# Optimization experiments

Hardware: AMD Instinct MI355X
Metric: run time of the kernel (lower is better)

Reference implementation:

```python
import jax, jax.numpy as jnp
import numpy as np

B = 32768          # batch (replay-buffer minibatch)
OBS, ACT = 17, 6   # HalfCheetah-style dims
IN = OBS + ACT
H = 256            # hidden width hard-coded in the module
N = 10             # num_q_nets


def setup_inputs() -> dict:
    key = jax.random.key(0)
    ks = jax.random.split(key, 8)
    # PyTorch Linear default init: U(-1/sqrt(fan_in), 1/sqrt(fan_in)); scale randn similarly.
    s1, s2, s3 = 1.0 / np.sqrt(IN), 1.0 / np.sqrt(H), 1.0 / np.sqrt(H)
    return {
        "state": jax.random.normal(ks[0], (B, OBS), dtype=jnp.float32),
        "action": jax.random.uniform(ks[1], (B, ACT), dtype=jnp.float32, minval=-1.0, maxval=1.0),
        "W1": jax.random.normal(ks[2], (N, IN, H), dtype=jnp.float32) * s1,
        "b1": jax.random.normal(ks[3], (N, H), dtype=jnp.float32) * s1,
        "W2": jax.random.normal(ks[4], (N, H, H), dtype=jnp.float32) * s2,
        "b2": jax.random.normal(ks[5], (N, H), dtype=jnp.float32) * s2,
        "W3": jax.random.normal(ks[6], (N, H, 1), dtype=jnp.float32) * s3,
        "b3": jax.random.normal(ks[7], (N, 1), dtype=jnp.float32) * s3,
    }


def reference(state, action, W1, b1, W2, b2, W3, b3):
    # x: [B, OBS+ACT]
    x = jnp.concatenate([state, action], axis=1)
    # batched-over-ensemble GEMMs; n=ensemble member, b=batch
    h1 = jax.nn.relu(jnp.einsum("bi,nih->nbh", x, W1) + b1[:, None, :])   # [N,B,H]
    h2 = jax.nn.relu(jnp.einsum("nbh,nho->nbo", h1, W2) + b2[:, None, :])  # [N,B,H]
    out = jnp.einsum("nbh,nho->nbo", h2, W3) + b3[:, None, :]              # [N,B,1]
    return out
```

## Files before the change

kernel.cpp:

```cpp
#include <hip/hip_runtime.h>
#include <hip/hip_bf16.h>


typedef __attribute__((ext_vector_type(8))) short bf16x8;
typedef __attribute__((ext_vector_type(4))) float f32x4;

#define B_TOTAL 32768
#define NQ 10
#define HDIM 256
#define BT 128
#define XS_STRIDE 40
#define H_STRIDE 264

#define W1P_ELEMS (NQ * 16 * 64 * 8)
#define W2P_ELEMS (NQ * 8 * 16 * 64 * 8)
#define W3P_ELEMS (NQ * 8 * 64 * 8)

__device__ __forceinline__ unsigned short f2bf(float f) {
  unsigned int u = __float_as_uint(f);
  u = u + 0x7FFFu + ((u >> 16) & 1u);
  return (unsigned short)(u >> 16);
}

__device__ __forceinline__ unsigned int pk2bf(float a, float b) {
  union { __hip_bfloat162 h; unsigned int u; } cv;
  cv.h = __float22bfloat162_rn(make_float2(a, b));
  return cv.u;
}

__global__ void pack_weights_kernel(const float* __restrict__ W1,
                                    const float* __restrict__ W2,
                                    const float* __restrict__ W3,
                                    unsigned short* __restrict__ w1p,
                                    unsigned short* __restrict__ w2p,
                                    unsigned short* __restrict__ w3p) {
  int t = blockIdx.x * 256 + threadIdx.x;
  const int NW1 = NQ * 16 * 64;
  const int NW2 = NQ * 8 * 16 * 64;
  if (t < NW1) {
    int lane = t & 63, mt = (t >> 6) & 15, n = t >> 10;
    int m = lane & 15, q = lane >> 4;
    int outc = mt * 16 + m;
#pragma unroll
    for (int j = 0; j < 8; j++) {
      int k = q * 8 + j;
      float v = (k < 23) ? W1[(n * 23 + k) * 256 + outc] : 0.f;
      w1p[(size_t)t * 8 + j] = f2bf(v);
    }
  } else if (t < NW1 + NW2) {
    int u = t - NW1;
    int lane = u & 63, mt = (u >> 6) & 15, kt = (u >> 10) & 7, n = u >> 13;
    int m = lane & 15, q = lane >> 4;
    int outc = mt * 16 + m;
#pragma unroll
    for (int j = 0; j < 8; j++) {
      int h = kt * 32 + q * 8 + j;
      w2p[(size_t)u * 8 + j] = f2bf(W2[((size_t)(n * 256 + h)) * 256 + outc]);
    }
  } else {
    int u = t - NW1 - NW2;
    int lane = u & 63, kt = (u >> 6) & 7, n = u >> 9;
    int m = lane & 15, q = lane >> 4;
#pragma unroll
    for (int j = 0; j < 8; j++) {
      int h = kt * 32 + q * 8 + j;
      float v = (m == 0) ? W3[n * 256 + h] : 0.f;
      w3p[(size_t)u * 8 + j] = f2bf(v);
    }
  }
}

__global__ __launch_bounds__(256, 2) void fused_ensemble_kernel(
    const float* __restrict__ state,
    const float* __restrict__ action,
    const unsigned short* __restrict__ w1p,
    const float* __restrict__ b1,
    const unsigned short* __restrict__ w2p,
    const float* __restrict__ b2,
    const unsigned short* __restrict__ w3p,
    const float* __restrict__ b3,
    float* __restrict__ out) {
  __shared__ __align__(16) unsigned short xs[BT * XS_STRIDE];
  __shared__ __align__(16) unsigned short hs[BT * H_STRIDE];

  const int tid = threadIdx.x;
  const int lane = tid & 63;
  const int wave = tid >> 6;
  const int m = lane & 15;
  const int q = lane >> 4;

  const int n = blockIdx.x >> 8;
  const int tile = blockIdx.x & 255;
  const int row0 = tile * BT;

  {
    const float* sp = state + (size_t)row0 * 17;
    for (int i = tid; i < BT * 17; i += 256) {
      int b = i / 17, k = i - b * 17;
      xs[b * XS_STRIDE + k] = f2bf(sp[i]);
    }
    const float* ap = action + (size_t)row0 * 6;
    for (int i = tid; i < BT * 6; i += 256) {
      int b = i / 6, k = i - b * 6;
      xs[b * XS_STRIDE + 17 + k] = f2bf(ap[i]);
    }
    for (int i = tid; i < BT * 9; i += 256) {
      int b = i / 9, k = i - b * 9;
      xs[b * XS_STRIDE + 23 + k] = 0;
    }
  }
  __syncthreads();

  f32x4 acc[4][8];

  {
    bf16x8 afrag[4];
#pragma unroll
    for (int mt = 0; mt < 4; mt++)
      afrag[mt] = *(const bf16x8*)(w1p + (((size_t)n * 16 + wave * 4 + mt) * 64 + lane) * 8);
#pragma unroll
    for (int mt = 0; mt < 4; mt++) {
      float4 bv = *(const float4*)&b1[n * HDIM + (wave * 4 + mt) * 16 + q * 4];
      f32x4 bi = (f32x4){bv.x, bv.y, bv.z, bv.w};
#pragma unroll
      for (int nt = 0; nt < 8; nt++) acc[mt][nt] = bi;
    }
#pragma unroll
    for (int nt = 0; nt < 8; nt++) {
      bf16x8 bfrag = *(const bf16x8*)&xs[(nt * 16 + m) * XS_STRIDE + q * 8];
#pragma unroll
      for (int mt = 0; mt < 4; mt++)
        acc[mt][nt] = __builtin_amdgcn_mfma_f32_16x16x32_bf16(afrag[mt], bfrag, acc[mt][nt], 0, 0, 0);
    }
  }

#pragma unroll
  for (int mt = 0; mt < 4; mt++)
#pragma unroll
    for (int nt = 0; nt < 8; nt++) {
      f32x4 a = acc[mt][nt];
      uint2 w;
      w.x = pk2bf(fmaxf(a[0], 0.f), fmaxf(a[1], 0.f));
      w.y = pk2bf(fmaxf(a[2], 0.f), fmaxf(a[3], 0.f));
      *(uint2*)&hs[(nt * 16 + m) * H_STRIDE + (wave * 4 + mt) * 16 + q * 4] = w;
    }
  __syncthreads();

  {
    const unsigned short* w2n = w2p + (size_t)n * (8 * 16 * 64 * 8);
    bf16x8 acur[4], anxt[4];
#pragma unroll
    for (int mt = 0; mt < 4; mt++)
      acur[mt] = *(const bf16x8*)(w2n + (((size_t)(wave * 4 + mt)) * 64 + lane) * 8);
#pragma unroll
    for (int mt = 0; mt < 4; mt++) {
      float4 bv = *(const float4*)&b2[n * HDIM + (wave * 4 + mt) * 16 + q * 4];
      f32x4 bi = (f32x4){bv.x, bv.y, bv.z, bv.w};
#pragma unroll
      for (int nt = 0; nt < 8; nt++) acc[mt][nt] = bi;
    }
#pragma unroll
    for (int kt = 0; kt < 8; kt++) {
      if (kt < 7) {
#pragma unroll
        for (int mt = 0; mt < 4; mt++)
          anxt[mt] = *(const bf16x8*)(w2n + (((size_t)(kt + 1) * 16 + wave * 4 + mt) * 64 + lane) * 8);
      }
      bf16x8 bfrag[8];
#pragma unroll
      for (int nt = 0; nt < 8; nt++)
        bfrag[nt] = *(const bf16x8*)&hs[(nt * 16 + m) * H_STRIDE + kt * 32 + q * 8];
#pragma unroll
      for (int nt = 0; nt < 8; nt++)
#pragma unroll
        for (int mt = 0; mt < 4; mt++)
          acc[mt][nt] = __builtin_amdgcn_mfma_f32_16x16x32_bf16(acur[mt], bfrag[nt], acc[mt][nt], 0, 0, 0);
#pragma unroll
      for (int mt = 0; mt < 4; mt++) acur[mt] = anxt[mt];
    }
  }
  __syncthreads();

#pragma unroll
  for (int mt = 0; mt < 4; mt++)
#pragma unroll
    for (int nt = 0; nt < 8; nt++) {
      f32x4 a = acc[mt][nt];
      uint2 w;
      w.x = pk2bf(fmaxf(a[0], 0.f), fmaxf(a[1], 0.f));
      w.y = pk2bf(fmaxf(a[2], 0.f), fmaxf(a[3], 0.f));
      *(uint2*)&hs[(nt * 16 + m) * H_STRIDE + (wave * 4 + mt) * 16 + q * 4] = w;
    }
  __syncthreads();

  {
    const unsigned short* w3n = w3p + (size_t)n * (8 * 64 * 8);
    f32x4 acc3[2];
    acc3[0] = (f32x4){0.f, 0.f, 0.f, 0.f};
    acc3[1] = (f32x4){0.f, 0.f, 0.f, 0.f};
#pragma unroll
    for (int kt = 0; kt < 8; kt++) {
      bf16x8 af = *(const bf16x8*)(w3n + ((size_t)kt * 64 + lane) * 8);
#pragma unroll
      for (int i = 0; i < 2; i++) {
        bf16x8 bf_ = *(const bf16x8*)&hs[((wave * 2 + i) * 16 + m) * H_STRIDE + kt * 32 + q * 8];
        acc3[i] = __builtin_amdgcn_mfma_f32_16x16x32_bf16(af, bf_, acc3[i], 0, 0, 0);
      }
    }
    if (lane < 16) {
      float bias = b3[n];
#pragma unroll
      for (int i = 0; i < 2; i++)
        out[(size_t)n * B_TOTAL + row0 + (wave * 2 + i) * 16 + m] = acc3[i][0] + bias;
    }
  }
}

extern "C" void kernel_launch(void* const* d_in, const int* in_sizes, int n_in,
                              void* d_out, int out_size, void* d_ws, size_t ws_size,
                              hipStream_t stream) {
  const float* state  = (const float*)d_in[0];
  const float* action = (const float*)d_in[1];
  const float* W1 = (const float*)d_in[2];
  const float* b1 = (const float*)d_in[3];
  const float* W2 = (const float*)d_in[4];
  const float* b2 = (const float*)d_in[5];
  const float* W3 = (const float*)d_in[6];
  const float* b3 = (const float*)d_in[7];
  float* out = (float*)d_out;

  unsigned short* w1p = (unsigned short*)d_ws;
  unsigned short* w2p = (unsigned short*)((char*)d_ws + (size_t)W1P_ELEMS * 2);
  unsigned short* w3p = (unsigned short*)((char*)d_ws + (size_t)(W1P_ELEMS + W2P_ELEMS) * 2);

  pack_weights_kernel<<<380, 256, 0, stream>>>(W1, W2, W3, w1p, w2p, w3p);
  fused_ensemble_kernel<<<NQ * (B_TOTAL / BT), 256, 0, stream>>>(
      state, action, w1p, b1, w2p, b2, w3p, b3, out);
}
```

Before: 132.5 us.

## Fuse layer-3 dot product into layer-2 epilogue and use 8 waves per block

Layer 3 is now computed straight from the layer-2 accumulators: ReLU, an FMA against fp32 W3, and a cross-lane plus cross-wave reduction through shared memory. This drops the second hidden-state write to LDS, its barrier, and the padded layer-3 MFMA pass. Blocks grow to 512 threads (8 waves, 2 M-tiles each), which halves the accumulator registers per wave and targets higher occupancy. The hidden LDS buffer uses a k-quad-major layout so that MFMA B-fragment reads are contiguous, and the pack kernel writes vectorized 16-byte stores and no longer packs W3.

```diff
diff --git a/kernel.cpp b/kernel.cpp
--- a/kernel.cpp
+++ b/kernel.cpp
@@ -10,11 +10,9 @@
 #define HDIM 256
 #define BT 128
 #define XS_STRIDE 40
-#define H_STRIDE 264
 
 #define W1P_ELEMS (NQ * 16 * 64 * 8)
 #define W2P_ELEMS (NQ * 8 * 16 * 64 * 8)
-#define W3P_ELEMS (NQ * 8 * 64 * 8)
 
 __device__ __forceinline__ unsigned short f2bf(float f) {
   unsigned int u = __float_as_uint(f);
@@ -30,131 +28,124 @@
 
 __global__ void pack_weights_kernel(const float* __restrict__ W1,
                                     const float* __restrict__ W2,
-                                    const float* __restrict__ W3,
                                     unsigned short* __restrict__ w1p,
-                                    unsigned short* __restrict__ w2p,
-                                    unsigned short* __restrict__ w3p) {
+                                    unsigned short* __restrict__ w2p) {
   int t = blockIdx.x * 256 + threadIdx.x;
   const int NW1 = NQ * 16 * 64;
-  const int NW2 = NQ * 8 * 16 * 64;
   if (t < NW1) {
     int lane = t & 63, mt = (t >> 6) & 15, n = t >> 10;
     int m = lane & 15, q = lane >> 4;
     int outc = mt * 16 + m;
+    unsigned short v[8];
 #pragma unroll
     for (int j = 0; j < 8; j++) {
       int k = q * 8 + j;
-      float v = (k < 23) ? W1[(n * 23 + k) * 256 + outc] : 0.f;
-      w1p[(size_t)t * 8 + j] = f2bf(v);
-    }
-  } else if (t < NW1 + NW2) {
+      v[j] = (k < 23) ? f2bf(W1[(n * 23 + k) * 256 + outc]) : (unsigned short)0;
+    }
+    *(uint4*)&w1p[(size_t)t * 8] = *(const uint4*)v;
+  } else {
     int u = t - NW1;
     int lane = u & 63, mt = (u >> 6) & 15, kt = (u >> 10) & 7, n = u >> 13;
     int m = lane & 15, q = lane >> 4;
     int outc = mt * 16 + m;
+    unsigned short v[8];
 #pragma unroll
     for (int j = 0; j < 8; j++) {
       int h = kt * 32 + q * 8 + j;
-      w2p[(size_t)u * 8 + j] = f2bf(W2[((size_t)(n * 256 + h)) * 256 + outc]);
-    }
-  } else {
-    int u = t - NW1 - NW2;
-    int lane = u & 63, kt = (u >> 6) & 7, n = u >> 9;
-    int m = lane & 15, q = lane >> 4;
-#pragma unroll
-    for (int j = 0; j < 8; j++) {
-      int h = kt * 32 + q * 8 + j;
-      float v = (m == 0) ? W3[n * 256 + h] : 0.f;
-      w3p[(size_t)u * 8 + j] = f2bf(v);
-    }
-  }
-}
-
-__global__ __launch_bounds__(256, 2) void fused_ensemble_kernel(
+      v[j] = f2bf(W2[((size_t)(n * 256 + h)) * 256 + outc]);
+    }
+    *(uint4*)&w2p[(size_t)u * 8] = *(const uint4*)v;
+  }
+}
+
+__global__ __launch_bounds__(512, 4) void fused_ensemble_kernel(
     const float* __restrict__ state,
     const float* __restrict__ action,
     const unsigned short* __restrict__ w1p,
     const float* __restrict__ b1,
     const unsigned short* __restrict__ w2p,
     const float* __restrict__ b2,
-    const unsigned short* __restrict__ w3p,
+    const float* __restrict__ W3,
     const float* __restrict__ b3,
     float* __restrict__ out) {
   __shared__ __align__(16) unsigned short xs[BT * XS_STRIDE];
-  __shared__ __align__(16) unsigned short hs[BT * H_STRIDE];
+  __shared__ __align__(16) unsigned short hs[32 * BT * 8];
 
   const int tid = threadIdx.x;
   const int lane = tid & 63;
-  const int wave = tid >> 6;
+  const int w = tid >> 6;
   const int m = lane & 15;
   const int q = lane >> 4;
 
   const int n = blockIdx.x >> 8;
-  const int tile = blockIdx.x & 255;
-  const int row0 = tile * BT;
+  const int row0 = (blockIdx.x & 255) * BT;
 
   {
     const float* sp = state + (size_t)row0 * 17;
-    for (int i = tid; i < BT * 17; i += 256) {
+    for (int i = tid; i < BT * 17; i += 512) {
       int b = i / 17, k = i - b * 17;
       xs[b * XS_STRIDE + k] = f2bf(sp[i]);
     }
     const float* ap = action + (size_t)row0 * 6;
-    for (int i = tid; i < BT * 6; i += 256) {
+    for (int i = tid; i < BT * 6; i += 512) {
       int b = i / 6, k = i - b * 6;
       xs[b * XS_STRIDE + 17 + k] = f2bf(ap[i]);
     }
-    for (int i = tid; i < BT * 9; i += 256) {
+    for (int i = tid; i < BT * 9; i += 512) {
       int b = i / 9, k = i - b * 9;
       xs[b * XS_STRIDE + 23 + k] = 0;
     }
   }
   __syncthreads();
 
-  f32x4 acc[4][8];
-
-  {
-    bf16x8 afrag[4];
-#pragma unroll
-    for (int mt = 0; mt < 4; mt++)
-      afrag[mt] = *(const bf16x8*)(w1p + (((size_t)n * 16 + wave * 4 + mt) * 64 + lane) * 8);
-#pragma unroll
-    for (int mt = 0; mt < 4; mt++) {
-      float4 bv = *(const float4*)&b1[n * HDIM + (wave * 4 + mt) * 16 + q * 4];
+  f32x4 acc[2][8];
+
+  {
+    bf16x8 af[2];
+#pragma unroll
+    for (int mt = 0; mt < 2; mt++)
+      af[mt] = *(const bf16x8*)(w1p + (((size_t)n * 16 + w * 2 + mt) * 64 + lane) * 8);
+#pragma unroll
+    for (int mt = 0; mt < 2; mt++) {
+      float4 bv = *(const float4*)&b1[n * HDIM + (w * 2 + mt) * 16 + q * 4];
       f32x4 bi = (f32x4){bv.x, bv.y, bv.z, bv.w};
 #pragma unroll
       for (int nt = 0; nt < 8; nt++) acc[mt][nt] = bi;
     }
 #pragma unroll
     for (int nt = 0; nt < 8; nt++) {
-      bf16x8 bfrag = *(const bf16x8*)&xs[(nt * 16 + m) * XS_STRIDE + q * 8];
-#pragma unroll
-      for (int mt = 0; mt < 4; mt++)
-        acc[mt][nt] = __builtin_amdgcn_mfma_f32_16x16x32_bf16(afrag[mt], bfrag, acc[mt][nt], 0, 0, 0);
-    }
-  }
-
-#pragma unroll
-  for (int mt = 0; mt < 4; mt++)
-#pragma unroll
-    for (int nt = 0; nt < 8; nt++) {
-      f32x4 a = acc[mt][nt];
-      uint2 w;
-      w.x = pk2bf(fmaxf(a[0], 0.f), fmaxf(a[1], 0.f));
-      w.y = pk2bf(fmaxf(a[2], 0.f), fmaxf(a[3], 0.f));
-      *(uint2*)&hs[(nt * 16 + m) * H_STRIDE + (wave * 4 + mt) * 16 + q * 4] = w;
-    }
+      bf16x8 bfr = *(const bf16x8*)&xs[(nt * 16 + m) * XS_STRIDE + q * 8];
+#pragma unroll
+      for (int mt = 0; mt < 2; mt++)
+        acc[mt][nt] = __builtin_amdgcn_mfma_f32_16x16x32_bf16(af[mt], bfr, acc[mt][nt], 0, 0, 0);
+    }
+  }
+
+  {
+    const int kqb = w * 4 + (q >> 1);
+    const int joff = (q & 1) * 4;
+#pragma unroll
+    for (int mt = 0; mt < 2; mt++)
+#pragma unroll
+      for (int nt = 0; nt < 8; nt++) {
+        f32x4 a = acc[mt][nt];
+        uint2 wv;
+        wv.x = pk2bf(fmaxf(a[0], 0.f), fmaxf(a[1], 0.f));
+        wv.y = pk2bf(fmaxf(a[2], 0.f), fmaxf(a[3], 0.f));
+        *(uint2*)&hs[(((kqb + mt * 2) * BT) + nt * 16 + m) * 8 + joff] = wv;
+      }
+  }
   __syncthreads();
 
   {
     const unsigned short* w2n = w2p + (size_t)n * (8 * 16 * 64 * 8);
-    bf16x8 acur[4], anxt[4];
-#pragma unroll
-    for (int mt = 0; mt < 4; mt++)
-      acur[mt] = *(const bf16x8*)(w2n + (((size_t)(wave * 4 + mt)) * 64 + lane) * 8);
-#pragma unroll
-    for (int mt = 0; mt < 4; mt++) {
-      float4 bv = *(const float4*)&b2[n * HDIM + (wave * 4 + mt) * 16 + q * 4];
+    bf16x8 acur[2], anxt[2];
+#pragma unroll
+    for (int mt = 0; mt < 2; mt++)
+      acur[mt] = *(const bf16x8*)(w2n + (((size_t)(w * 2 + mt)) * 64 + lane) * 8);
+#pragma unroll
+    for (int mt = 0; mt < 2; mt++) {
+      float4 bv = *(const float4*)&b2[n * HDIM + (w * 2 + mt) * 16 + q * 4];
       f32x4 bi = (f32x4){bv.x, bv.y, bv.z, bv.w};
 #pragma unroll
       for (int nt = 0; nt < 8; nt++) acc[mt][nt] = bi;
@@ -163,55 +154,62 @@
     for (int kt = 0; kt < 8; kt++) {
       if (kt < 7) {
 #pragma unroll
-        for (int mt = 0; mt < 4; mt++)
-          anxt[mt] = *(const bf16x8*)(w2n + (((size_t)(kt + 1) * 16 + wave * 4 + mt) * 64 + lane) * 8);
-      }
-      bf16x8 bfrag[8];
-#pragma unroll
-      for (int nt = 0; nt < 8; nt++)
-        bfrag[nt] = *(const bf16x8*)&hs[(nt * 16 + m) * H_STRIDE + kt * 32 + q * 8];
-#pragma unroll
-      for (int nt = 0; nt < 8; nt++)
-#pragma unroll
-        for (int mt = 0; mt < 4; mt++)
-          acc[mt][nt] = __builtin_amdgcn_mfma_f32_16x16x32_bf16(acur[mt], bfrag[nt], acc[mt][nt], 0, 0, 0);
-#pragma unroll
-      for (int mt = 0; mt < 4; mt++) acur[mt] = anxt[mt];
-    }
-  }
-  __syncthreads();
-
-#pragma unroll
-  for (int mt = 0; mt < 4; mt++)
+        for (int mt = 0; mt < 2; mt++)
+          anxt[mt] = *(const bf16x8*)(w2n + (((size_t)(kt + 1) * 16 + w * 2 + mt) * 64 + lane) * 8);
+      }
+#pragma unroll
+      for (int half = 0; half < 2; half++) {
+        bf16x8 bfr[4];
+#pragma unroll
+        for (int i = 0; i < 4; i++) {
+          int nt = half * 4 + i;
+          bfr[i] = *(const bf16x8*)&hs[((kt * 4 + q) * BT + nt * 16 + m) * 8];
+        }
+#pragma unroll
+        for (int i = 0; i < 4; i++)
+#pragma unroll
+          for (int mt = 0; mt < 2; mt++)
+            acc[mt][half * 4 + i] = __builtin_amdgcn_mfma_f32_16x16x32_bf16(
+                acur[mt], bfr[i], acc[mt][half * 4 + i], 0, 0, 0);
+      }
+#pragma unroll
+      for (int mt = 0; mt < 2; mt++) acur[mt] = anxt[mt];
+    }
+  }
+
+  {
+    float4 w3v[2];
+#pragma unroll
+    for (int mt = 0; mt < 2; mt++)
+      w3v[mt] = *(const float4*)&W3[n * HDIM + (w * 2 + mt) * 16 + q * 4];
+    float p[8];
 #pragma unroll
     for (int nt = 0; nt < 8; nt++) {
-      f32x4 a = acc[mt][nt];
-      uint2 w;
-      w.x = pk2bf(fmaxf(a[0], 0.f), fmaxf(a[1], 0.f));
-      w.y = pk2bf(fmaxf(a[2], 0.f), fmaxf(a[3], 0.f));
-      *(uint2*)&hs[(nt * 16 + m) * H_STRIDE + (wave * 4 + mt) * 16 + q * 4] = w;
-    }
-  __syncthreads();
-
-  {
-    const unsigned short* w3n = w3p + (size_t)n * (8 * 64 * 8);
-    f32x4 acc3[2];
-    acc3[0] = (f32x4){0.f, 0.f, 0.f, 0.f};
-    acc3[1] = (f32x4){0.f, 0.f, 0.f, 0.f};
-#pragma unroll
-    for (int kt = 0; kt < 8; kt++) {
-      bf16x8 af = *(const bf16x8*)(w3n + ((size_t)kt * 64 + lane) * 8);
-#pragma unroll
-      for (int i = 0; i < 2; i++) {
-        bf16x8 bf_ = *(const bf16x8*)&hs[((wave * 2 + i) * 16 + m) * H_STRIDE + kt * 32 + q * 8];
-        acc3[i] = __builtin_amdgcn_mfma_f32_16x16x32_bf16(af, bf_, acc3[i], 0, 0, 0);
-      }
-    }
-    if (lane < 16) {
-      float bias = b3[n];
-#pragma unroll
-      for (int i = 0; i < 2; i++)
-        out[(size_t)n * B_TOTAL + row0 + (wave * 2 + i) * 16 + m] = acc3[i][0] + bias;
+      float s = 0.f;
+#pragma unroll
+      for (int mt = 0; mt < 2; mt++) {
+        f32x4 a = acc[mt][nt];
+        float4 wv = w3v[mt];
+        s = fmaf(fmaxf(a[0], 0.f), wv.x, s);
+        s = fmaf(fmaxf(a[1], 0.f), wv.y, s);
+        s = fmaf(fmaxf(a[2], 0.f), wv.z, s);
+        s = fmaf(fmaxf(a[3], 0.f), wv.w, s);
+      }
+      s += __shfl_xor(s, 16, 64);
+      s += __shfl_xor(s, 32, 64);
+      p[nt] = s;
+    }
+    float* red = (float*)xs;
+    if (q == 0) {
+#pragma unroll
+      for (int nt = 0; nt < 8; nt++) red[w * BT + nt * 16 + m] = p[nt];
+    }
+    __syncthreads();
+    if (tid < BT) {
+      float s = b3[n];
+#pragma unroll
+      for (int ww = 0; ww < 8; ww++) s += red[ww * BT + tid];
+      out[(size_t)n * B_TOTAL + row0 + tid] = s;
     }
   }
 }
@@ -231,9 +229,8 @@
 
   unsigned short* w1p = (unsigned short*)d_ws;
   unsigned short* w2p = (unsigned short*)((char*)d_ws + (size_t)W1P_ELEMS * 2);
-  unsigned short* w3p = (unsigned short*)((char*)d_ws + (size_t)(W1P_ELEMS + W2P_ELEMS) * 2);
-
-  pack_weights_kernel<<<380, 256, 0, stream>>>(W1, W2, W3, w1p, w2p, w3p);
-  fused_ensemble_kernel<<<NQ * (B_TOTAL / BT), 256, 0, stream>>>(
-      state, action, w1p, b1, w2p, b2, w3p, b3, out);
-}
+
+  pack_weights_kernel<<<360, 256, 0, stream>>>(W1, W2, w1p, w2p);
+  fused_ensemble_kernel<<<NQ * (B_TOTAL / BT), 512, 0, stream>>>(
+      state, action, w1p, b1, w2p, b2, W3, b3, out);
+}
```

Result: faster. 120.8 us (-8.8%).
